# Kernel tuning notes

Measured on AMD Instinct MI355X. Metric: run time of the kernel, lower is better.

Reference implementation:

```python
import jax, jax.numpy as jnp
import numpy as np

_BN_EPS = 1e-5
_BN_SCALE = 1.0 / np.sqrt(1.0 + _BN_EPS)  # eval-mode BN with running mean 0, var 1

def _gelu(x):
    return jax.nn.gelu(x, approximate=False)

def _ln(x, w, b, eps):
    mu = jnp.mean(x, -1, keepdims=True)
    v = jnp.mean((x - mu) ** 2, -1, keepdims=True)
    return (x - mu) * jax.lax.rsqrt(v + eps) * w + b

def _bn(x, s, b):  # NCHW eval BatchNorm (running_mean=0, running_var=1)
    return x * (s * _BN_SCALE)[None, :, None, None] + b[None, :, None, None]

def _conv(x, w, stride=1, pad=1, groups=1, bias=None):
    y = jax.lax.conv_general_dilated(x, w, (stride, stride), [(pad, pad), (pad, pad)],
                                     feature_group_count=groups,
                                     dimension_numbers=('NCHW', 'OIHW', 'NCHW'))
    return y if bias is None else y + bias[None, :, None, None]

def _selective_scan(u, delta, A, Bs, Cs):
    # u, delta: (B,K,D,L); A: (K,D,N); Bs, Cs: (B,K,N,L) -> y: (B,K,D,L)
    def step(h, inp):
        u_l, d_l, B_l, C_l = inp
        dA = jnp.exp(d_l[..., None] * A)                       # (B,K,D,N)
        h = dA * h + (d_l * u_l)[..., None] * B_l[:, :, None, :]
        return h, jnp.sum(h * C_l[:, :, None, :], axis=-1)
    h0 = jnp.zeros(u.shape[:-1] + (A.shape[-1],), u.dtype)
    ins = tuple(jnp.moveaxis(t, -1, 0) for t in (u, delta, Bs, Cs))
    _, ys = jax.lax.scan(step, h0, ins)
    return jnp.moveaxis(ys, 0, -1)

def _ss2d(xh, in_proj, conv_w, conv_b, xproj, dtw, dtb, Alog, D, onw, onb, outproj):
    # xh: (B,H,W,C) -> (B,H,W,C); VMamba SS2D forward_corev0 (4-direction cross-scan)
    B, H, W, C = xh.shape
    di = conv_w.shape[0]
    L = H * W
    xz = xh @ in_proj.T                                        # (B,H,W,2*di)
    xm, z = jnp.split(xz, 2, axis=-1)
    xm = jax.nn.silu(_conv(xm.transpose(0, 3, 1, 2), conv_w, pad=1, groups=di, bias=conv_b))
    x1 = xm.reshape(B, di, L)                                  # row-major scan
    x2 = xm.transpose(0, 1, 3, 2).reshape(B, di, L)            # column-major scan
    xs = jnp.stack([x1, x2, x1[..., ::-1], x2[..., ::-1]], axis=1)  # (B,4,di,L)
    x_dbl = jnp.einsum('bkdl,kcd->bkcl', xs, xproj)
    R = dtw.shape[-1]; N = Alog.shape[-1]
    dts, Bm, Cm = jnp.split(x_dbl, [R, R + N], axis=2)
    delta = jax.nn.softplus(jnp.einsum('bkrl,kdr->bkdl', dts, dtw) + dtb[None, :, :, None])
    A = -jnp.exp(Alog)
    ys = _selective_scan(xs, delta, A, Bm, Cm) + D[None, :, :, None] * xs
    inv = ys[:, 2:4, :, ::-1]
    wh = ys[:, 1].reshape(B, di, W, H).transpose(0, 1, 3, 2).reshape(B, di, L)
    invwh = inv[:, 1].reshape(B, di, W, H).transpose(0, 1, 3, 2).reshape(B, di, L)
    y = ys[:, 0] + inv[:, 0] + wh + invwh                      # (B,di,L)
    y = _ln(y.transpose(0, 2, 1).reshape(B, H, W, di), onw, onb, 1e-5)
    return (y * jax.nn.silu(z)) @ outproj.T

def _forward(x, vss_ln_w, vss_ln_b, vss_in_proj, vss_conv_w, vss_conv_b, vss_xproj, vss_dtw, vss_dtb, vss_Alog, vss_D, vss_onw, vss_onb, vss_outproj, ds_dw, ds_bn1s, ds_bn1b, ds_pw, ds_bn2s, ds_bn2b, fus_c1, fus_bn1s, fus_bn1b, fus_c2, fus_bn2s, fus_bn2b, op_bn0s, op_bn0b, op_conv, op_bn1s, op_bn1b):
    vssp = (vss_ln_w, vss_ln_b, vss_in_proj, vss_conv_w, vss_conv_b, vss_xproj,
            vss_dtw, vss_dtb, vss_Alog, vss_D, vss_onw, vss_onb, vss_outproj)
    def vss(xc, i):  # NCHW -> NHWC -> VSSBlock (x + SS2D(LN(x)), drop_path=identity in eval) -> NCHW
        p = [a[i] for a in vssp]
        xh = xc.transpose(0, 2, 3, 1)
        out = xh + _ss2d(_ln(xh, p[0], p[1], 1e-6), *p[2:])
        return out.transpose(0, 3, 1, 2)
    def down(xc, j):  # depthwise stride-2 conv + BN + GELU, then pointwise conv + BN + GELU
        h = _gelu(_bn(_conv(xc, ds_dw[j], stride=2, pad=1, groups=xc.shape[1]), ds_bn1s[j], ds_bn1b[j]))
        return _gelu(_bn(_conv(h, ds_pw[j], pad=0), ds_bn2s[j], ds_bn2b[j]))
    def resblk(xc, j):  # conv-BN-GELU-(dropout eval=id)-conv-BN + identity, GELU
        h = _gelu(_bn(_conv(xc, fus_c1[j]), fus_bn1s[j], fus_bn1b[j]))
        h = _bn(_conv(h, fus_c2[j]), fus_bn2s[j], fus_bn2b[j])
        return _gelu(h + xc)
    def up(xc, Ho, Wo):  # bilinear, align_corners=True
        h, w = xc.shape[2], xc.shape[3]
        ys = jnp.linspace(0.0, h - 1.0, Ho); xs_ = jnp.linspace(0.0, w - 1.0, Wo)
        y0 = jnp.floor(ys).astype(jnp.int32); y1 = jnp.minimum(y0 + 1, h - 1); wy = (ys - y0).astype(xc.dtype)
        x0 = jnp.floor(xs_).astype(jnp.int32); x1 = jnp.minimum(x0 + 1, w - 1); wx = (xs_ - x0).astype(xc.dtype)
        g = xc[:, :, y0, :] * (1 - wy)[None, None, :, None] + xc[:, :, y1, :] * wy[None, None, :, None]
        return g[:, :, :, x0] * (1 - wx) + g[:, :, :, x1] * wx
    identity = x
    xr = vss(vss(x, 0), 1)                                    # initial refinement
    pyr = [xr]
    cur = xr
    for j in range(2):                                        # pyramid: 16x16 -> 8x8 -> 4x4
        cur = down(cur, j)
        pyr.append(cur)
    proc = [vss(pyr[k], 2 + k) for k in range(3)]             # scale-specific Mamba
    fused = proc[2]
    for i in (1, 0):                                          # bottom-up fusion
        upf = up(fused, proc[i].shape[2], proc[i].shape[3])
        fused = resblk(proc[i] + upf, 1 - i)
    h = _gelu(_bn(fused, op_bn0s, op_bn0b))
    out = _gelu(_bn(_conv(h, op_conv, pad=1), op_bn1s, op_bn1b))
    return out + identity

def setup_inputs() -> dict:
    key = jax.random.key(0)
    ks = iter(jax.random.split(key, 64))
    f32 = jnp.float32
    C, DI, K, N, R = 512, 1024, 4, 16, 32
    B, H, W = 4, 16, 16
    def rn(shape, s=0.02):
        return jax.random.normal(next(ks), shape, f32) * s
    return dict(
        x=jax.random.normal(next(ks), (B, C, H, W), f32),
        vss_ln_w=jnp.ones((5, C), f32), vss_ln_b=jnp.zeros((5, C), f32),
        vss_in_proj=rn((5, 2 * DI, C), 0.03),
        vss_conv_w=rn((5, DI, 1, 3, 3), 0.1), vss_conv_b=jnp.zeros((5, DI), f32),
        vss_xproj=rn((5, K, R + 2 * N, DI), 0.02),
        vss_dtw=rn((5, K, DI, R), 0.05),
        vss_dtb=jax.random.uniform(next(ks), (5, K, DI), f32, -4.0, -2.0),
        vss_Alog=jnp.broadcast_to(jnp.log(jnp.arange(1.0, N + 1.0, dtype=f32)), (5, K, DI, N)).copy(),
        vss_D=jnp.ones((5, K, DI), f32),
        vss_onw=jnp.ones((5, DI), f32), vss_onb=jnp.zeros((5, DI), f32),
        vss_outproj=rn((5, C, DI), 0.02),
        ds_dw=rn((2, C, 1, 3, 3), 0.1), ds_bn1s=jnp.ones((2, C), f32), ds_bn1b=jnp.zeros((2, C), f32),
        ds_pw=rn((2, C, C, 1, 1), 0.03), ds_bn2s=jnp.ones((2, C), f32), ds_bn2b=jnp.zeros((2, C), f32),
        fus_c1=rn((2, C, C, 3, 3), 0.01), fus_bn1s=jnp.ones((2, C), f32), fus_bn1b=jnp.zeros((2, C), f32),
        fus_c2=rn((2, C, C, 3, 3), 0.01), fus_bn2s=jnp.ones((2, C), f32), fus_bn2b=jnp.zeros((2, C), f32),
        op_bn0s=jnp.ones((C,), f32), op_bn0b=jnp.zeros((C,), f32),
        op_conv=rn((C, C, 3, 3), 0.01),
        op_bn1s=jnp.ones((C,), f32), op_bn1b=jnp.zeros((C,), f32),
    )

def reference(x, vss_ln_w, vss_ln_b, vss_in_proj, vss_conv_w, vss_conv_b, vss_xproj, vss_dtw, vss_dtb, vss_Alog, vss_D, vss_onw, vss_onb, vss_outproj, ds_dw, ds_bn1s, ds_bn1b, ds_pw, ds_bn2s, ds_bn2b, fus_c1, fus_bn1s, fus_bn1b, fus_c2, fus_bn2s, fus_bn2b, op_bn0s, op_bn0b, op_conv, op_bn1s, op_bn1b):
    return _forward(x, vss_ln_w, vss_ln_b, vss_in_proj, vss_conv_w, vss_conv_b, vss_xproj, vss_dtw, vss_dtb, vss_Alog, vss_D, vss_onw, vss_onb, vss_outproj, ds_dw, ds_bn1s, ds_bn1b, ds_pw, ds_bn2s, ds_bn2b, fus_c1, fus_bn1s, fus_bn1b, fus_c2, fus_bn2s, fus_bn2b, op_bn0s, op_bn0b, op_conv, op_bn1s, op_bn1b)
```

## Files before the change

### kernel.cpp

```cpp
#include <hip/hip_runtime.h>
#include <hip/hip_bf16.h>
#include <math.h>


constexpr int B_  = 4;
constexpr int C_  = 512;
constexpr int DI_ = 1024;
constexpr int K_  = 4;
constexpr int N_  = 16;
constexpr int R_  = 32;
constexpr int KC9 = C_ * 9;
constexpr int KSPL = 4;
constexpr int KSEG = KC9 / KSPL;
constexpr float BNS_ = 0.9999950000374997f;

typedef __attribute__((ext_vector_type(8))) short bf16x8;
typedef __attribute__((ext_vector_type(4))) float f32x4;

__device__ inline float geluf(float x) {
    return 0.5f * x * (1.0f + erff(x * 0.70710678118654752f));
}
__device__ inline float siluf(float x) {
    return x / (1.0f + expf(-x));
}
__device__ inline float softplusf(float x) {
    return fmaxf(x, 0.0f) + log1pf(expf(-fabsf(x)));
}
__device__ inline float softplus_fast(float x) {
    return fmaxf(x, 0.0f) + __logf(1.0f + __expf(-fabsf(x)));
}
__device__ inline short bf16s(float x) {
    __hip_bfloat16 h = __float2bfloat16(x);
    return *reinterpret_cast<short*>(&h);
}

__device__ inline float blockReduceSum(float v, float* sd) {
    int tid = threadIdx.x;
    sd[tid] = v; __syncthreads();
    for (int s = blockDim.x / 2; s > 0; s >>= 1) {
        if (tid < s) sd[tid] += sd[tid + s];
        __syncthreads();
    }
    float r = sd[0]; __syncthreads();
    return r;
}

__global__ void k_ln_nchw(const float* __restrict__ x, const float* __restrict__ w,
                          const float* __restrict__ b, float* __restrict__ out,
                          int L, float eps) {
    int row = blockIdx.x;
    int bb = row / L, l = row % L;
    __shared__ float sd[256];
    __shared__ float srow[C_];
    const float* xp = x + (size_t)bb * C_ * L + l;
    float sum = 0.f;
    for (int c = threadIdx.x; c < C_; c += 256) { float v = xp[(size_t)c * L]; srow[c] = v; sum += v; }
    sum = blockReduceSum(sum, sd);
    float mu = sum / C_;
    float vs = 0.f;
    for (int c = threadIdx.x; c < C_; c += 256) { float d = srow[c] - mu; vs += d * d; }
    vs = blockReduceSum(vs, sd);
    float rstd = rsqrtf(vs / C_ + eps);
    float* op = out + (size_t)row * C_;
    for (int c = threadIdx.x; c < C_; c += 256) op[c] = (srow[c] - mu) * rstd * w[c] + b[c];
}

template <int EPI>
__global__ void k_gemm_mfma(const float* __restrict__ A, const float* __restrict__ Bw,
                            float* __restrict__ Cout, int M, int Nn, int Kk,
                            const float* __restrict__ Res, int L) {
    const int BK = 32, PITCH = 40;
    __shared__ short As[64 * PITCH];
    __shared__ short Bs[64 * PITCH];
    int m0 = blockIdx.y * 64, n0 = blockIdx.x * 64;
    int tid = threadIdx.x;
    int wv = tid >> 6, lane = tid & 63;
    int frow = lane & 15, kg = lane >> 4;
    f32x4 acc[4];
#pragma unroll
    for (int t = 0; t < 4; t++) acc[t] = (f32x4){0.f, 0.f, 0.f, 0.f};

    int sr = tid >> 2;
    int kq = (tid & 3) * 4;
    for (int k0 = 0; k0 < Kk; k0 += BK) {
        const float* ap = A + (size_t)(m0 + sr) * Kk + k0;
        const float* bp = Bw + (size_t)(n0 + sr) * Kk + k0;
        float4 a1 = *reinterpret_cast<const float4*>(ap + kq);
        float4 a2 = *reinterpret_cast<const float4*>(ap + kq + 16);
        float4 b1 = *reinterpret_cast<const float4*>(bp + kq);
        float4 b2 = *reinterpret_cast<const float4*>(bp + kq + 16);
        short* ad = &As[sr * PITCH + kq];
        ad[0] = bf16s(a1.x); ad[1] = bf16s(a1.y); ad[2] = bf16s(a1.z); ad[3] = bf16s(a1.w);
        ad[16] = bf16s(a2.x); ad[17] = bf16s(a2.y); ad[18] = bf16s(a2.z); ad[19] = bf16s(a2.w);
        short* bd = &Bs[sr * PITCH + kq];
        bd[0] = bf16s(b1.x); bd[1] = bf16s(b1.y); bd[2] = bf16s(b1.z); bd[3] = bf16s(b1.w);
        bd[16] = bf16s(b2.x); bd[17] = bf16s(b2.y); bd[18] = bf16s(b2.z); bd[19] = bf16s(b2.w);
        __syncthreads();
        bf16x8 afrag = *reinterpret_cast<const bf16x8*>(&As[(wv * 16 + frow) * PITCH + kg * 8]);
#pragma unroll
        for (int t = 0; t < 4; t++) {
            bf16x8 bfrag = *reinterpret_cast<const bf16x8*>(&Bs[(t * 16 + frow) * PITCH + kg * 8]);
            acc[t] = __builtin_amdgcn_mfma_f32_16x16x32_bf16(afrag, bfrag, acc[t], 0, 0, 0);
        }
        __syncthreads();
    }

    int orow = kg * 4;
#pragma unroll
    for (int t = 0; t < 4; t++) {
#pragma unroll
        for (int r = 0; r < 4; r++) {
            int m = m0 + wv * 16 + orow + r;
            int n = n0 + t * 16 + frow;
            if (EPI == 0) {
                Cout[(size_t)m * Nn + n] = acc[t][r];
            } else {
                int bb = m / L, l = m % L;
                size_t o = ((size_t)bb * C_ + n) * L + l;
                Cout[o] = Res[o] + acc[t][r];
            }
        }
    }
}

__global__ void k_gemm_part(const float* __restrict__ A, const float* __restrict__ Bw,
                            float* __restrict__ partial, int M, int Nn, int Kk) {
    const int BK = 32, PITCH = 40;
    __shared__ short As[64 * PITCH];
    __shared__ short Bs[64 * PITCH];
    int m0 = blockIdx.y * 64, n0 = blockIdx.x * 64;
    int s = blockIdx.z;
    int tid = threadIdx.x;
    int wv = tid >> 6, lane = tid & 63;
    int frow = lane & 15, kg = lane >> 4;
    f32x4 acc[4];
#pragma unroll
    for (int t = 0; t < 4; t++) acc[t] = (f32x4){0.f, 0.f, 0.f, 0.f};

    int sr = tid >> 2;
    int kq = (tid & 3) * 4;
    int kseg = Kk / KSPL;
    int kbeg = s * kseg;
    for (int k0 = kbeg; k0 < kbeg + kseg; k0 += BK) {
        const float* ap = A + (size_t)(m0 + sr) * Kk + k0;
        const float* bp = Bw + (size_t)(n0 + sr) * Kk + k0;
        float4 a1 = *reinterpret_cast<const float4*>(ap + kq);
        float4 a2 = *reinterpret_cast<const float4*>(ap + kq + 16);
        float4 b1 = *reinterpret_cast<const float4*>(bp + kq);
        float4 b2 = *reinterpret_cast<const float4*>(bp + kq + 16);
        short* ad = &As[sr * PITCH + kq];
        ad[0] = bf16s(a1.x); ad[1] = bf16s(a1.y); ad[2] = bf16s(a1.z); ad[3] = bf16s(a1.w);
        ad[16] = bf16s(a2.x); ad[17] = bf16s(a2.y); ad[18] = bf16s(a2.z); ad[19] = bf16s(a2.w);
        short* bd = &Bs[sr * PITCH + kq];
        bd[0] = bf16s(b1.x); bd[1] = bf16s(b1.y); bd[2] = bf16s(b1.z); bd[3] = bf16s(b1.w);
        bd[16] = bf16s(b2.x); bd[17] = bf16s(b2.y); bd[18] = bf16s(b2.z); bd[19] = bf16s(b2.w);
        __syncthreads();
        bf16x8 afrag = *reinterpret_cast<const bf16x8*>(&As[(wv * 16 + frow) * PITCH + kg * 8]);
#pragma unroll
        for (int t = 0; t < 4; t++) {
            bf16x8 bfrag = *reinterpret_cast<const bf16x8*>(&Bs[(t * 16 + frow) * PITCH + kg * 8]);
            acc[t] = __builtin_amdgcn_mfma_f32_16x16x32_bf16(afrag, bfrag, acc[t], 0, 0, 0);
        }
        __syncthreads();
    }

    int orow = kg * 4;
    float* pb = partial + (size_t)s * M * Nn;
#pragma unroll
    for (int t = 0; t < 4; t++) {
#pragma unroll
        for (int r = 0; r < 4; r++) {
            int m = m0 + wv * 16 + orow + r;
            int n = n0 + t * 16 + frow;
            pb[(size_t)m * Nn + n] = acc[t][r];
        }
    }
}

__global__ void k_outproj_fin(const float* __restrict__ partial, const float* __restrict__ res,
                              float* __restrict__ out, int L) {
    int Nn = C_;
    int total = B_ * L * Nn;
    int idx = blockIdx.x * 256 + threadIdx.x;
    if (idx >= total) return;
    int m = idx / Nn, n = idx % Nn;
    float a = 0.f;
#pragma unroll
    for (int s = 0; s < KSPL; s++) a += partial[(size_t)s * B_ * L * Nn + idx];
    int bb = m / L, l = m % L;
    size_t o = ((size_t)bb * C_ + n) * L + l;
    out[o] = res[o] + a;
}

__global__ void k_im2col(const float* __restrict__ inp, short* __restrict__ ocol,
                         int H, int W) {
    int L = H * W;
    int total = B_ * L * KC9;
    int idx = blockIdx.x * 256 + threadIdx.x;
    if (idx >= total) return;
    int kidx = idx % KC9; int n = idx / KC9;
    int ci = kidx / 9; int q = kidx % 9;
    int dy = q / 3, dx = q % 3;
    int l = n % L; int bb = n / L;
    int h = l / W, w = l % W;
    int hh = h + dy - 1, ww = w + dx - 1;
    float v = 0.f;
    if ((unsigned)hh < (unsigned)H && (unsigned)ww < (unsigned)W)
        v = inp[(((size_t)bb * C_ + ci) * H + hh) * W + ww];
    ocol[idx] = bf16s(v);
}

__global__ void k_gemm_conv_part(const float* __restrict__ wgt, const short* __restrict__ bcol,
                                 float* __restrict__ partial, int Nn) {
    const int BK = 32, PITCH = 40;
    __shared__ short As[64 * PITCH];
    __shared__ short Bs[64 * PITCH];
    int m0 = blockIdx.y * 64, n0 = blockIdx.x * 64;
    int s = blockIdx.z;
    int tid = threadIdx.x;
    int wv = tid >> 6, lane = tid & 63;
    int frow = lane & 15, kg = lane >> 4;
    f32x4 acc[4];
#pragma unroll
    for (int t = 0; t < 4; t++) acc[t] = (f32x4){0.f, 0.f, 0.f, 0.f};

    int sr = tid >> 2;
    int kq = (tid & 3) * 4;
    int kq8 = (tid & 3) * 8;
    int kbeg = s * KSEG;
    for (int k0 = kbeg; k0 < kbeg + KSEG; k0 += BK) {
        const float* ap = wgt + (size_t)(m0 + sr) * KC9 + k0;
        float4 a1 = *reinterpret_cast<const float4*>(ap + kq);
        float4 a2 = *reinterpret_cast<const float4*>(ap + kq + 16);
        short* ad = &As[sr * PITCH + kq];
        ad[0] = bf16s(a1.x); ad[1] = bf16s(a1.y); ad[2] = bf16s(a1.z); ad[3] = bf16s(a1.w);
        ad[16] = bf16s(a2.x); ad[17] = bf16s(a2.y); ad[18] = bf16s(a2.z); ad[19] = bf16s(a2.w);
        uint4 bv = *reinterpret_cast<const uint4*>(bcol + (size_t)(n0 + sr) * KC9 + k0 + kq8);
        *reinterpret_cast<uint4*>(&Bs[sr * PITCH + kq8]) = bv;
        __syncthreads();
        bf16x8 afrag = *reinterpret_cast<const bf16x8*>(&As[(wv * 16 + frow) * PITCH + kg * 8]);
#pragma unroll
        for (int t = 0; t < 4; t++) {
            bf16x8 bfrag = *reinterpret_cast<const bf16x8*>(&Bs[(t * 16 + frow) * PITCH + kg * 8]);
            acc[t] = __builtin_amdgcn_mfma_f32_16x16x32_bf16(afrag, bfrag, acc[t], 0, 0, 0);
        }
        __syncthreads();
    }

    int orow = kg * 4;
    float* pb = partial + (size_t)s * C_ * Nn;
#pragma unroll
    for (int t = 0; t < 4; t++) {
#pragma unroll
        for (int r = 0; r < 4; r++) {
            int m = m0 + wv * 16 + orow + r;
            int n = n0 + t * 16 + frow;
            pb[(size_t)m * Nn + n] = acc[t][r];
        }
    }
}

template <int CM>
__global__ void k_conv_fin2(const float* __restrict__ partial, const float* __restrict__ bns,
                            const float* __restrict__ bnb, const float* __restrict__ res,
                            float* __restrict__ out, int Nn, int L) {
    int idx = blockIdx.x * 256 + threadIdx.x;
    int total = C_ * Nn;
    if (idx >= total) return;
    int m = idx / Nn, n = idx % Nn;
    float a = 0.f;
#pragma unroll
    for (int s = 0; s < KSPL; s++) a += partial[(size_t)s * C_ * Nn + idx];
    int bb = n / L, l = n % L;
    size_t o = ((size_t)bb * C_ + m) * L + l;
    a = a * (bns[m] * BNS_) + bnb[m];
    if (CM == 0) out[o] = geluf(a);
    else if (CM == 1) out[o] = geluf(a + res[o]);
    else out[o] = geluf(a) + res[o];
}

__global__ void k_dwconv_silu(const float* __restrict__ xz, const float* __restrict__ cw,
                              const float* __restrict__ cb, float* __restrict__ xm,
                              float* __restrict__ xmT, int H, int W) {
    int L = H * W;
    int idx = blockIdx.x * 256 + threadIdx.x;
    int total = B_ * L * DI_;
    if (idx >= total) return;
    int d = idx % DI_; int t = idx / DI_; int l = t % L; int bb = t / L;
    int h = l / W, w = l % W;
    float acc = cb[d];
    const float* wp = cw + d * 9;
#pragma unroll
    for (int dy = 0; dy < 3; dy++) {
        int hh = h + dy - 1;
        if ((unsigned)hh >= (unsigned)H) continue;
#pragma unroll
        for (int dx = 0; dx < 3; dx++) {
            int ww = w + dx - 1;
            if ((unsigned)ww >= (unsigned)W) continue;
            acc += xz[((size_t)bb * L + hh * W + ww) * (2 * DI_) + d] * wp[dy * 3 + dx];
        }
    }
    float v = siluf(acc);
    xm[idx] = v;
    xmT[((size_t)bb * DI_ + d) * L + l] = v;
}

__device__ inline int dir_src(int k, int l, int H, int W, int L) {
    int ll = (k >= 2) ? (L - 1 - l) : l;
    return (k & 1) ? ((ll % H) * W + ll / H) : ll;
}

__global__ void k_gather_xdbl(const float* __restrict__ tmp, float* __restrict__ xdbl,
                              int H, int W) {
    int L = H * W;
    int Nn = B_ * L;
    int total = B_ * K_ * 64 * L;
    int idx = blockIdx.x * 256 + threadIdx.x;
    if (idx >= total) return;
    int l = idx % L; int t = idx / L; int c = t % 64; t /= 64; int k = t % K_; int bb = t / K_;
    int src = dir_src(k, l, H, W, L);
    size_t col = (size_t)bb * L + src;
    float v = 0.f;
#pragma unroll
    for (int s = 0; s < KSPL; s++)
        v += tmp[((size_t)s * K_ * 64 + k * 64 + c) * Nn + col];
    xdbl[idx] = v;
}

template <int LT>
__global__ void k_scan_wave(const float* __restrict__ xmT, const float* __restrict__ xdbl,
                            const float* __restrict__ dtw, const float* __restrict__ dtb,
                            const float* __restrict__ Alog, const float* __restrict__ Dp,
                            float* __restrict__ part, int H, int W) {
    constexpr int SPL = (LT == 256) ? 4 : 1;
    constexpr int CW  = (LT < 64) ? LT : 64;
    const int L = LT;
    int lane = threadIdx.x & 63;
    int wv = threadIdx.x >> 6;
    int blk = blockIdx.x;
    const int ndq = DI_ / 4;
    int dq = blk % ndq; int t2 = blk / ndq; int k = t2 % K_; int bb = t2 / K_;
    int d = dq * 4 + wv;

    const float* wrow = dtw + ((size_t)k * DI_ + d) * R_;
    const float* al   = Alog + ((size_t)k * DI_ + d) * N_;
    float bias = dtb[k * DI_ + d];
    float Dv   = Dp[k * DI_ + d];

    const float* bc = xdbl + (size_t)(bb * K_ + k) * 64 * L;
    const float* ut = xmT + ((size_t)bb * DI_ + d) * L;
    float* yb = part + (size_t)(bb * K_ + k) * L * DI_ + d;

    int lj = lane < CW ? lane : CW - 1;
    int base = lj * SPL;

    float dl[SPL], du[SPL], uu[SPL], y[SPL];
    {
        float accv[SPL];
#pragma unroll
        for (int i = 0; i < SPL; i++) accv[i] = bias;
#pragma unroll 8
        for (int r = 0; r < R_; r++) {
            float wr = wrow[r];
            if constexpr (SPL == 4) {
                float4 d4 = *reinterpret_cast<const float4*>(bc + (size_t)r * L + base);
                accv[0] += d4.x * wr; accv[1] += d4.y * wr;
                accv[2] += d4.z * wr; accv[3] += d4.w * wr;
            } else {
                accv[0] += bc[(size_t)r * L + base] * wr;
            }
        }
#pragma unroll
        for (int i = 0; i < SPL; i++) {
            int src = dir_src(k, base + i, H, W, L);
            dl[i] = softplus_fast(accv[i]);
            uu[i] = ut[src];
            du[i] = dl[i] * uu[i];
            y[i] = 0.f;
        }
    }

#pragma unroll 1
    for (int n = 0; n < N_; n++) {
        float An = -__expf(al[n]);
        float aL, bL;
        if constexpr (SPL == 4) {
            float4 B4 = *reinterpret_cast<const float4*>(bc + (size_t)(R_ + n) * L + base);
            float a0 = __expf(dl[0] * An);
            float a1 = __expf(dl[1] * An);
            float a2 = __expf(dl[2] * An);
            float a3 = __expf(dl[3] * An);
            aL = a0; bL = du[0] * B4.x;
            bL = a1 * bL + du[1] * B4.y; aL = a1 * aL;
            bL = a2 * bL + du[2] * B4.z; aL = a2 * aL;
            bL = a3 * bL + du[3] * B4.w; aL = a3 * aL;
#pragma unroll
            for (int off = 1; off < CW; off <<= 1) {
                float ap = __shfl_up(aL, off);
                float bp = __shfl_up(bL, off);
                if (lane >= off) { bL = aL * bp + bL; aL = aL * ap; }
            }
            float hin = __shfl_up(bL, 1);
            if (lane == 0) hin = 0.f;
            float4 C4 = *reinterpret_cast<const float4*>(bc + (size_t)(R_ + N_ + n) * L + base);
            float h = hin;
            h = a0 * h + du[0] * B4.x; y[0] += h * C4.x;
            h = a1 * h + du[1] * B4.y; y[1] += h * C4.y;
            h = a2 * h + du[2] * B4.z; y[2] += h * C4.z;
            h = a3 * h + du[3] * B4.w; y[3] += h * C4.w;
        } else {
            float Bv = bc[(size_t)(R_ + n) * L + base];
            float a0 = __expf(dl[0] * An);
            aL = a0;
            bL = du[0] * Bv;
#pragma unroll
            for (int off = 1; off < CW; off <<= 1) {
                float ap = __shfl_up(aL, off);
                float bp = __shfl_up(bL, off);
                if (lane >= off) { bL = aL * bp + bL; aL = aL * ap; }
            }
            float hin = __shfl_up(bL, 1);
            if (lane == 0) hin = 0.f;
            float h = a0 * hin + du[0] * Bv;
            y[0] += h * bc[(size_t)(R_ + N_ + n) * L + base];
        }
    }

    if (lane < CW) {
#pragma unroll
        for (int i = 0; i < SPL; i++) {
            int src = dir_src(k, base + i, H, W, L);
            yb[(size_t)src * DI_] = y[i] + Dv * uu[i];
        }
    }
}

__global__ void k_merge_ln_silu(const float* __restrict__ part, const float* __restrict__ xz,
                                const float* __restrict__ onw, const float* __restrict__ onb,
                                float* __restrict__ tout, int L) {
    int row = blockIdx.x;
    int bb = row / L, l = row % L;
    __shared__ float sd[256];
    __shared__ float srow[DI_];
    const float* p0 = part + ((size_t)(bb * K_ + 0) * L + l) * DI_;
    const float* p1 = part + ((size_t)(bb * K_ + 1) * L + l) * DI_;
    const float* p2 = part + ((size_t)(bb * K_ + 2) * L + l) * DI_;
    const float* p3 = part + ((size_t)(bb * K_ + 3) * L + l) * DI_;
    float sum = 0.f;
    for (int d = threadIdx.x; d < DI_; d += 256) {
        float v = p0[d] + p1[d] + p2[d] + p3[d];
        srow[d] = v; sum += v;
    }
    sum = blockReduceSum(sum, sd);
    float mu = sum / DI_;
    float vs = 0.f;
    for (int d = threadIdx.x; d < DI_; d += 256) { float dv = srow[d] - mu; vs += dv * dv; }
    vs = blockReduceSum(vs, sd);
    float rstd = rsqrtf(vs / DI_ + 1e-5f);
    const float* zp = xz + (size_t)row * 2 * DI_ + DI_;
    float* tp = tout + (size_t)row * DI_;
    for (int d = threadIdx.x; d < DI_; d += 256) {
        float zn = zp[d];
        tp[d] = ((srow[d] - mu) * rstd * onw[d] + onb[d]) * siluf(zn);
    }
}

__global__ void k_dwconv_s2_bn_gelu(const float* __restrict__ x, const float* __restrict__ dw,
                                    const float* __restrict__ bns, const float* __restrict__ bnb,
                                    float* __restrict__ out, int Hi, int Wi) {
    int Ho = Hi / 2, Wo = Wi / 2;
    int idx = blockIdx.x * 256 + threadIdx.x;
    int total = B_ * C_ * Ho * Wo;
    if (idx >= total) return;
    int wo = idx % Wo; int t = idx / Wo; int ho = t % Ho; t /= Ho; int c = t % C_; int bb = t / C_;
    float acc = 0.f;
    const float* xp = x + ((size_t)bb * C_ + c) * Hi * Wi;
    const float* wp = dw + c * 9;
#pragma unroll
    for (int dy = 0; dy < 3; dy++) {
        int ih = ho * 2 + dy - 1;
        if ((unsigned)ih >= (unsigned)Hi) continue;
#pragma unroll
        for (int dx = 0; dx < 3; dx++) {
            int iw = wo * 2 + dx - 1;
            if ((unsigned)iw >= (unsigned)Wi) continue;
            acc += xp[ih * Wi + iw] * wp[dy * 3 + dx];
        }
    }
    acc = acc * (bns[c] * BNS_) + bnb[c];
    out[idx] = geluf(acc);
}

__global__ void k_pwconv_bn_gelu(const float* __restrict__ x, const float* __restrict__ pw,
                                 const float* __restrict__ bns, const float* __restrict__ bnb,
                                 float* __restrict__ out, int L) {
    int idx = blockIdx.x * 256 + threadIdx.x;
    int total = B_ * C_ * L;
    if (idx >= total) return;
    int l = idx % L; int t = idx / L; int co = t % C_; int bb = t / C_;
    const float* xp = x + (size_t)bb * C_ * L + l;
    const float* wp = pw + (size_t)co * C_;
    float acc = 0.f;
    for (int ci = 0; ci < C_; ci++) acc += xp[(size_t)ci * L] * wp[ci];
    acc = acc * (bns[co] * BNS_) + bnb[co];
    out[idx] = geluf(acc);
}

__global__ void k_up_add(const float* __restrict__ low, const float* __restrict__ skip,
                         float* __restrict__ out, int Hi, int Wi, int Ho, int Wo) {
    int idx = blockIdx.x * 256 + threadIdx.x;
    int total = B_ * C_ * Ho * Wo;
    if (idx >= total) return;
    int wo = idx % Wo; int t = idx / Wo; int ho = t % Ho; t /= Ho; int c = t % C_; int bb = t / C_;
    float fy = (float)ho * (float)(Hi - 1) / (float)(Ho - 1);
    float fx = (float)wo * (float)(Wi - 1) / (float)(Wo - 1);
    int y0 = (int)floorf(fy); int y1 = min(y0 + 1, Hi - 1); float wy = fy - (float)y0;
    int x0 = (int)floorf(fx); int x1 = min(x0 + 1, Wi - 1); float wx = fx - (float)x0;
    const float* lp = low + ((size_t)bb * C_ + c) * Hi * Wi;
    float g0 = lp[y0 * Wi + x0] * (1.f - wy) + lp[y1 * Wi + x0] * wy;
    float g1 = lp[y0 * Wi + x1] * (1.f - wy) + lp[y1 * Wi + x1] * wy;
    out[idx] = skip[idx] + g0 * (1.f - wx) + g1 * wx;
}

__global__ void k_bn_gelu(const float* __restrict__ x, const float* __restrict__ s,
                          const float* __restrict__ b, float* __restrict__ out, int L) {
    int idx = blockIdx.x * 256 + threadIdx.x;
    int total = B_ * C_ * L;
    if (idx >= total) return;
    int t = idx / L; int c = t % C_;
    out[idx] = geluf(x[idx] * (s[c] * BNS_) + b[c]);
}

__global__ void k_fill_out(float* o, int n, float v) {
    int i = blockIdx.x * 256 + threadIdx.x;
    if (i < n) o[i] = v;
}

struct VssW {
    const float *lnw, *lnb, *inproj, *convw, *convb, *xproj, *dtw, *dtb, *Alog, *D, *onw, *onb, *outproj;
};

static void run_vss(const float* xc_in, float* xc_out, const VssW& p, int H, int W,
                    float* xln, float* xz, float* xm, float* xmT, float* xdbl,
                    float* part, float* ybuf, float* tbuf, float* cpart2,
                    hipStream_t stream) {
    int L = H * W, M = B_ * L;
    k_ln_nchw<<<M, 256, 0, stream>>>(xc_in, p.lnw, p.lnb, xln, L, 1e-6f);
    {
        dim3 g(2 * DI_ / 64, M / 64);
        k_gemm_mfma<0><<<g, 256, 0, stream>>>(xln, p.inproj, xz, M, 2 * DI_, C_, nullptr, L);
    }
    {
        int tot = B_ * L * DI_;
        k_dwconv_silu<<<(tot + 255) / 256, 256, 0, stream>>>(xz, p.convw, p.convb, xm, xmT, H, W);
    }
    {
        float* tmp = ybuf;
        dim3 g(M / 64, (K_ * 64) / 64, KSPL);
        k_gemm_part<<<g, 256, 0, stream>>>(p.xproj, xm, tmp, K_ * 64, M, DI_);
        int tot = B_ * K_ * 64 * L;
        k_gather_xdbl<<<(tot + 255) / 256, 256, 0, stream>>>(tmp, xdbl, H, W);
    }
    {
        int g = B_ * K_ * (DI_ / 4);
        if (L == 256)
            k_scan_wave<256><<<g, 256, 0, stream>>>(xmT, xdbl, p.dtw, p.dtb, p.Alog, p.D, part, H, W);
        else if (L == 64)
            k_scan_wave<64><<<g, 256, 0, stream>>>(xmT, xdbl, p.dtw, p.dtb, p.Alog, p.D, part, H, W);
        else
            k_scan_wave<16><<<g, 256, 0, stream>>>(xmT, xdbl, p.dtw, p.dtb, p.Alog, p.D, part, H, W);
    }
    k_merge_ln_silu<<<M, 256, 0, stream>>>(part, xz, p.onw, p.onb, tbuf, L);
    {
        dim3 g(C_ / 64, M / 64, KSPL);
        k_gemm_part<<<g, 256, 0, stream>>>(tbuf, p.outproj, cpart2, M, C_, DI_);
        int tot = M * C_;
        k_outproj_fin<<<(tot + 255) / 256, 256, 0, stream>>>(cpart2, xc_in, xc_out, L);
    }
}

extern "C" void kernel_launch(void* const* d_in, const int* in_sizes, int n_in,
                              void* d_out, int out_size, void* d_ws, size_t ws_size,
                              hipStream_t stream) {
    constexpr size_t NEED_FLOATS = 14221312;
    constexpr size_t NEED_BYTES  = NEED_FLOATS * 4;
    if (ws_size < NEED_BYTES) {
        k_fill_out<<<(out_size + 255) / 256, 256, 0, stream>>>((float*)d_out, out_size, 0.0f);
        return;
    }

    const float* x        = (const float*)d_in[0];
    const float* lnw      = (const float*)d_in[1];
    const float* lnb      = (const float*)d_in[2];
    const float* inproj   = (const float*)d_in[3];
    const float* convw    = (const float*)d_in[4];
    const float* convb    = (const float*)d_in[5];
    const float* xprojp   = (const float*)d_in[6];
    const float* dtwp     = (const float*)d_in[7];
    const float* dtbp     = (const float*)d_in[8];
    const float* Alogp    = (const float*)d_in[9];
    const float* Dpp      = (const float*)d_in[10];
    const float* onwp     = (const float*)d_in[11];
    const float* onbp     = (const float*)d_in[12];
    const float* outprojp = (const float*)d_in[13];
    const float* ds_dw    = (const float*)d_in[14];
    const float* ds_bn1s  = (const float*)d_in[15];
    const float* ds_bn1b  = (const float*)d_in[16];
    const float* ds_pw    = (const float*)d_in[17];
    const float* ds_bn2s  = (const float*)d_in[18];
    const float* ds_bn2b  = (const float*)d_in[19];
    const float* fus_c1   = (const float*)d_in[20];
    const float* fus_bn1s = (const float*)d_in[21];
    const float* fus_bn1b = (const float*)d_in[22];
    const float* fus_c2   = (const float*)d_in[23];
    const float* fus_bn2s = (const float*)d_in[24];
    const float* fus_bn2b = (const float*)d_in[25];
    const float* op_bn0s  = (const float*)d_in[26];
    const float* op_bn0b  = (const float*)d_in[27];
    const float* op_conv  = (const float*)d_in[28];
    const float* op_bn1s  = (const float*)d_in[29];
    const float* op_bn1b  = (const float*)d_in[30];

    float* ws = (float*)d_ws;
    float* xln   = ws;
    float* xz    = ws + 524288;
    float* xm    = ws + 2621440;
    float* xdbl  = ws + 3670016;
    float* ybuf  = ws + 3932160;
    float* part  = ws + 4980736;
    float* tbuf  = part;
    float* t_a   = ws + 9175040;
    float* xr    = ws + 9699328;
    float* p1    = ws + 10223616;
    float* p2    = ws + 10354688;
    float* proc0 = ws + 10387456;
    float* proc1 = ws + 10911744;
    float* proc2 = ws + 11042816;
    float* xmT   = ws + 11075584;
    float* cpart2= ws + 12124160;
    tbuf = ybuf;
    float* p1pre = xz;
    float* p2pre = xz + 131072;
    float* up1t  = xln;
    float* rbh1  = xln + 131072;
    float* fus1  = xln + 262144;
    float* up0t  = xm;
    float* rbh0  = part;
    float* fus0  = part + 524288;
    float* hbuf  = part + 1048576;
    short* icol = (short*)(ws + 6553600);

    VssW vp[5];
    for (int i = 0; i < 5; i++) {
        vp[i].lnw     = lnw + (size_t)i * C_;
        vp[i].lnb     = lnb + (size_t)i * C_;
        vp[i].inproj  = inproj + (size_t)i * 2 * DI_ * C_;
        vp[i].convw   = convw + (size_t)i * DI_ * 9;
        vp[i].convb   = convb + (size_t)i * DI_;
        vp[i].xproj   = xprojp + (size_t)i * K_ * 64 * DI_;
        vp[i].dtw     = dtwp + (size_t)i * K_ * DI_ * R_;
        vp[i].dtb     = dtbp + (size_t)i * K_ * DI_;
        vp[i].Alog    = Alogp + (size_t)i * K_ * DI_ * N_;
        vp[i].D       = Dpp + (size_t)i * K_ * DI_;
        vp[i].onw     = onwp + (size_t)i * DI_;
        vp[i].onb     = onbp + (size_t)i * DI_;
        vp[i].outproj = outprojp + (size_t)i * C_ * DI_;
    }

    run_vss(x,   t_a, vp[0], 16, 16, xln, xz, xm, xmT, xdbl, part, ybuf, tbuf, cpart2, stream);
    run_vss(t_a, xr,  vp[1], 16, 16, xln, xz, xm, xmT, xdbl, part, ybuf, tbuf, cpart2, stream);

    k_dwconv_s2_bn_gelu<<<(B_ * C_ * 64 + 255) / 256, 256, 0, stream>>>(
        xr, ds_dw, ds_bn1s, ds_bn1b, p1pre, 16, 16);
    k_pwconv_bn_gelu<<<(B_ * C_ * 64 + 255) / 256, 256, 0, stream>>>(
        p1pre, ds_pw, ds_bn2s, ds_bn2b, p1, 64);
    k_dwconv_s2_bn_gelu<<<(B_ * C_ * 16 + 255) / 256, 256, 0, stream>>>(
        p1, ds_dw + (size_t)C_ * 9, ds_bn1s + C_, ds_bn1b + C_, p2pre, 8, 8);
    k_pwconv_bn_gelu<<<(B_ * C_ * 16 + 255) / 256, 256, 0, stream>>>(
        p2pre, ds_pw + (size_t)C_ * C_, ds_bn2s + C_, ds_bn2b + C_, p2, 16);

    run_vss(xr, proc0, vp[2], 16, 16, xln, xz, xm, xmT, xdbl, part, ybuf, tbuf, cpart2, stream);
    run_vss(p1, proc1, vp[3],  8,  8, xln, xz, xm, xmT, xdbl, part, ybuf, tbuf, cpart2, stream);
    run_vss(p2, proc2, vp[4],  4,  4, xln, xz, xm, xmT, xdbl, part, ybuf, tbuf, cpart2, stream);

    k_up_add<<<(B_ * C_ * 64 + 255) / 256, 256, 0, stream>>>(proc2, proc1, up1t, 4, 4, 8, 8);
    {
        int Nn = B_ * 64;
        int tot = Nn * KC9;
        int tfin = C_ * Nn;
        dim3 gg(Nn / 64, C_ / 64, KSPL);
        k_im2col<<<(tot + 255) / 256, 256, 0, stream>>>(up1t, icol, 8, 8);
        k_gemm_conv_part<<<gg, 256, 0, stream>>>(fus_c1, icol, cpart2, Nn);
        k_conv_fin2<0><<<(tfin + 255) / 256, 256, 0, stream>>>(cpart2, fus_bn1s, fus_bn1b,
                                                               nullptr, rbh1, Nn, 64);
        k_im2col<<<(tot + 255) / 256, 256, 0, stream>>>(rbh1, icol, 8, 8);
        k_gemm_conv_part<<<gg, 256, 0, stream>>>(fus_c2, icol, cpart2, Nn);
        k_conv_fin2<1><<<(tfin + 255) / 256, 256, 0, stream>>>(cpart2, fus_bn2s, fus_bn2b,
                                                               up1t, fus1, Nn, 64);
    }
    k_up_add<<<(B_ * C_ * 256 + 255) / 256, 256, 0, stream>>>(fus1, proc0, up0t, 8, 8, 16, 16);
    {
        int Nn = B_ * 256;
        int tot = Nn * KC9;
        int tfin = C_ * Nn;
        dim3 gg(Nn / 64, C_ / 64, KSPL);
        k_im2col<<<(tot + 255) / 256, 256, 0, stream>>>(up0t, icol, 16, 16);
        k_gemm_conv_part<<<gg, 256, 0, stream>>>(fus_c1 + (size_t)C_ * KC9, icol, cpart2, Nn);
        k_conv_fin2<0><<<(tfin + 255) / 256, 256, 0, stream>>>(cpart2, fus_bn1s + C_, fus_bn1b + C_,
                                                               nullptr, rbh0, Nn, 256);
        k_im2col<<<(tot + 255) / 256, 256, 0, stream>>>(rbh0, icol, 16, 16);
        k_gemm_conv_part<<<gg, 256, 0, stream>>>(fus_c2 + (size_t)C_ * KC9, icol, cpart2, Nn);
        k_conv_fin2<1><<<(tfin + 255) / 256, 256, 0, stream>>>(cpart2, fus_bn2s + C_, fus_bn2b + C_,
                                                               up0t, fus0, Nn, 256);
    }

    k_bn_gelu<<<(B_ * C_ * 256 + 255) / 256, 256, 0, stream>>>(fus0, op_bn0s, op_bn0b, hbuf, 256);
    {
        int Nn = B_ * 256;
        int tot = Nn * KC9;
        int tfin = C_ * Nn;
        dim3 gg(Nn / 64, C_ / 64, KSPL);
        k_im2col<<<(tot + 255) / 256, 256, 0, stream>>>(hbuf, icol, 16, 16);
        k_gemm_conv_part<<<gg, 256, 0, stream>>>(op_conv, icol, cpart2, Nn);
        k_conv_fin2<2><<<(tfin + 255) / 256, 256, 0, stream>>>(cpart2, op_bn1s, op_bn1b,
                                                               x, (float*)d_out, Nn, 256);
    }
    (void)in_sizes; (void)n_in; (void)out_size;
}
```

Measured before the change: 834.5 us.

## Route pointwise downsample convs through MFMA split-K GEMM and fuse final BN-GELU

The depthwise stride-2 conv now writes channel-last (token-major) output so the following 1x1 pointwise conv can run on the existing split-K k_gemm_part MFMA GEMM. A new k_pw_fin kernel sums the partials, applies BN and GELU, and writes NCHW. This replaces the naive scalar per-output dot-product kernel, which was slow. Separately, the op-head BN+GELU is folded into the last fusion conv's epilogue (new CM==3 mode), which removes one elementwise pass and its intermediate buffer.

```diff
diff --git a/kernel.cpp b/kernel.cpp
--- a/kernel.cpp
+++ b/kernel.cpp
@@ -192,6 +192,20 @@
     out[o] = res[o] + a;
 }
 
+__global__ void k_pw_fin(const float* __restrict__ partial, const float* __restrict__ bns,
+                         const float* __restrict__ bnb, float* __restrict__ out,
+                         int M, int L2) {
+    int total = M * C_;
+    int idx = blockIdx.x * 256 + threadIdx.x;
+    if (idx >= total) return;
+    int m = idx / C_, n = idx % C_;
+    float a = 0.f;
+#pragma unroll
+    for (int s = 0; s < KSPL; s++) a += partial[(size_t)s * M * C_ + idx];
+    int bb = m / L2, l = m % L2;
+    out[((size_t)bb * C_ + n) * L2 + l] = geluf(a * (bns[n] * BNS_) + bnb[n]);
+}
+
 __global__ void k_im2col(const float* __restrict__ inp, short* __restrict__ ocol,
                          int H, int W) {
     int L = H * W;
@@ -263,7 +277,8 @@
 template <int CM>
 __global__ void k_conv_fin2(const float* __restrict__ partial, const float* __restrict__ bns,
                             const float* __restrict__ bnb, const float* __restrict__ res,
-                            float* __restrict__ out, int Nn, int L) {
+                            float* __restrict__ out, int Nn, int L,
+                            const float* __restrict__ bns2, const float* __restrict__ bnb2) {
     int idx = blockIdx.x * 256 + threadIdx.x;
     int total = C_ * Nn;
     if (idx >= total) return;
@@ -276,7 +291,37 @@
     a = a * (bns[m] * BNS_) + bnb[m];
     if (CM == 0) out[o] = geluf(a);
     else if (CM == 1) out[o] = geluf(a + res[o]);
-    else out[o] = geluf(a) + res[o];
+    else if (CM == 2) out[o] = geluf(a) + res[o];
+    else {
+        float v = geluf(a + res[o]);
+        out[o] = geluf(v * (bns2[m] * BNS_) + bnb2[m]);
+    }
+}
+
+__global__ void k_dwconv_s2_bn_gelu(const float* __restrict__ x, const float* __restrict__ dw,
+                                    const float* __restrict__ bns, const float* __restrict__ bnb,
+                                    float* __restrict__ out, int Hi, int Wi) {
+    int Ho = Hi / 2, Wo = Wi / 2;
+    int idx = blockIdx.x * 256 + threadIdx.x;
+    int total = B_ * C_ * Ho * Wo;
+    if (idx >= total) return;
+    int c = idx % C_; int t = idx / C_; int wo = t % Wo; t /= Wo; int ho = t % Ho; int bb = t / Ho;
+    float acc = 0.f;
+    const float* xp = x + ((size_t)bb * C_ + c) * Hi * Wi;
+    const float* wp = dw + c * 9;
+#pragma unroll
+    for (int dy = 0; dy < 3; dy++) {
+        int ih = ho * 2 + dy - 1;
+        if ((unsigned)ih >= (unsigned)Hi) continue;
+#pragma unroll
+        for (int dx = 0; dx < 3; dx++) {
+            int iw = wo * 2 + dx - 1;
+            if ((unsigned)iw >= (unsigned)Wi) continue;
+            acc += xp[ih * Wi + iw] * wp[dy * 3 + dx];
+        }
+    }
+    acc = acc * (bns[c] * BNS_) + bnb[c];
+    out[((size_t)(bb * Ho + ho) * Wo + wo) * C_ + c] = geluf(acc);
 }
 
 __global__ void k_dwconv_silu(const float* __restrict__ xz, const float* __restrict__ cw,
@@ -466,47 +511,6 @@
     }
 }
 
-__global__ void k_dwconv_s2_bn_gelu(const float* __restrict__ x, const float* __restrict__ dw,
-                                    const float* __restrict__ bns, const float* __restrict__ bnb,
-                                    float* __restrict__ out, int Hi, int Wi) {
-    int Ho = Hi / 2, Wo = Wi / 2;
-    int idx = blockIdx.x * 256 + threadIdx.x;
-    int total = B_ * C_ * Ho * Wo;
-    if (idx >= total) return;
-    int wo = idx % Wo; int t = idx / Wo; int ho = t % Ho; t /= Ho; int c = t % C_; int bb = t / C_;
-    float acc = 0.f;
-    const float* xp = x + ((size_t)bb * C_ + c) * Hi * Wi;
-    const float* wp = dw + c * 9;
-#pragma unroll
-    for (int dy = 0; dy < 3; dy++) {
-        int ih = ho * 2 + dy - 1;
-        if ((unsigned)ih >= (unsigned)Hi) continue;
-#pragma unroll
-        for (int dx = 0; dx < 3; dx++) {
-            int iw = wo * 2 + dx - 1;
-            if ((unsigned)iw >= (unsigned)Wi) continue;
-            acc += xp[ih * Wi + iw] * wp[dy * 3 + dx];
-        }
-    }
-    acc = acc * (bns[c] * BNS_) + bnb[c];
-    out[idx] = geluf(acc);
-}
-
-__global__ void k_pwconv_bn_gelu(const float* __restrict__ x, const float* __restrict__ pw,
-                                 const float* __restrict__ bns, const float* __restrict__ bnb,
-                                 float* __restrict__ out, int L) {
-    int idx = blockIdx.x * 256 + threadIdx.x;
-    int total = B_ * C_ * L;
-    if (idx >= total) return;
-    int l = idx % L; int t = idx / L; int co = t % C_; int bb = t / C_;
-    const float* xp = x + (size_t)bb * C_ * L + l;
-    const float* wp = pw + (size_t)co * C_;
-    float acc = 0.f;
-    for (int ci = 0; ci < C_; ci++) acc += xp[(size_t)ci * L] * wp[ci];
-    acc = acc * (bns[co] * BNS_) + bnb[co];
-    out[idx] = geluf(acc);
-}
-
 __global__ void k_up_add(const float* __restrict__ low, const float* __restrict__ skip,
                          float* __restrict__ out, int Hi, int Wi, int Ho, int Wo) {
     int idx = blockIdx.x * 256 + threadIdx.x;
@@ -521,15 +525,6 @@
     float g0 = lp[y0 * Wi + x0] * (1.f - wy) + lp[y1 * Wi + x0] * wy;
     float g1 = lp[y0 * Wi + x1] * (1.f - wy) + lp[y1 * Wi + x1] * wy;
     out[idx] = skip[idx] + g0 * (1.f - wx) + g1 * wx;
-}
-
-__global__ void k_bn_gelu(const float* __restrict__ x, const float* __restrict__ s,
-                          const float* __restrict__ b, float* __restrict__ out, int L) {
-    int idx = blockIdx.x * 256 + threadIdx.x;
-    int total = B_ * C_ * L;
-    if (idx >= total) return;
-    int t = idx / L; int c = t % C_;
-    out[idx] = geluf(x[idx] * (s[c] * BNS_) + b[c]);
 }
 
 __global__ void k_fill_out(float* o, int n, float v) {
@@ -640,14 +635,13 @@
     float* xmT   = ws + 11075584;
     float* cpart2= ws + 12124160;
     tbuf = ybuf;
-    float* p1pre = xz;
-    float* p2pre = xz + 131072;
+    float* p1preT= xz;
+    float* p2preT= xz + 131072;
     float* up1t  = xln;
     float* rbh1  = xln + 131072;
     float* fus1  = xln + 262144;
     float* up0t  = xm;
     float* rbh0  = part;
-    float* fus0  = part + 524288;
     float* hbuf  = part + 1048576;
     short* icol = (short*)(ws + 6553600);
 
@@ -672,13 +666,21 @@
     run_vss(t_a, xr,  vp[1], 16, 16, xln, xz, xm, xmT, xdbl, part, ybuf, tbuf, cpart2, stream);
 
     k_dwconv_s2_bn_gelu<<<(B_ * C_ * 64 + 255) / 256, 256, 0, stream>>>(
-        xr, ds_dw, ds_bn1s, ds_bn1b, p1pre, 16, 16);
-    k_pwconv_bn_gelu<<<(B_ * C_ * 64 + 255) / 256, 256, 0, stream>>>(
-        p1pre, ds_pw, ds_bn2s, ds_bn2b, p1, 64);
+        xr, ds_dw, ds_bn1s, ds_bn1b, p1preT, 16, 16);
+    {
+        int M = B_ * 64;
+        dim3 g(C_ / 64, M / 64, KSPL);
+        k_gemm_part<<<g, 256, 0, stream>>>(p1preT, ds_pw, cpart2, M, C_, C_);
+        k_pw_fin<<<(M * C_ + 255) / 256, 256, 0, stream>>>(cpart2, ds_bn2s, ds_bn2b, p1, M, 64);
+    }
     k_dwconv_s2_bn_gelu<<<(B_ * C_ * 16 + 255) / 256, 256, 0, stream>>>(
-        p1, ds_dw + (size_t)C_ * 9, ds_bn1s + C_, ds_bn1b + C_, p2pre, 8, 8);
-    k_pwconv_bn_gelu<<<(B_ * C_ * 16 + 255) / 256, 256, 0, stream>>>(
-        p2pre, ds_pw + (size_t)C_ * C_, ds_bn2s + C_, ds_bn2b + C_, p2, 16);
+        p1, ds_dw + (size_t)C_ * 9, ds_bn1s + C_, ds_bn1b + C_, p2preT, 8, 8);
+    {
+        int M = B_ * 16;
+        dim3 g(C_ / 64, M / 64, KSPL);
+        k_gemm_part<<<g, 256, 0, stream>>>(p2preT, ds_pw + (size_t)C_ * C_, cpart2, M, C_, C_);
+        k_pw_fin<<<(M * C_ + 255) / 256, 256, 0, stream>>>(cpart2, ds_bn2s + C_, ds_bn2b + C_, p2, M, 16);
+    }
 
     run_vss(xr, proc0, vp[2], 16, 16, xln, xz, xm, xmT, xdbl, part, ybuf, tbuf, cpart2, stream);
     run_vss(p1, proc1, vp[3],  8,  8, xln, xz, xm, xmT, xdbl, part, ybuf, tbuf, cpart2, stream);
@@ -693,11 +695,13 @@
         k_im2col<<<(tot + 255) / 256, 256, 0, stream>>>(up1t, icol, 8, 8);
         k_gemm_conv_part<<<gg, 256, 0, stream>>>(fus_c1, icol, cpart2, Nn);
         k_conv_fin2<0><<<(tfin + 255) / 256, 256, 0, stream>>>(cpart2, fus_bn1s, fus_bn1b,
-                                                               nullptr, rbh1, Nn, 64);
+                                                               nullptr, rbh1, Nn, 64,
+                                                               nullptr, nullptr);
         k_im2col<<<(tot + 255) / 256, 256, 0, stream>>>(rbh1, icol, 8, 8);
         k_gemm_conv_part<<<gg, 256, 0, stream>>>(fus_c2, icol, cpart2, Nn);
         k_conv_fin2<1><<<(tfin + 255) / 256, 256, 0, stream>>>(cpart2, fus_bn2s, fus_bn2b,
-                                                               up1t, fus1, Nn, 64);
+                                                               up1t, fus1, Nn, 64,
+                                                               nullptr, nullptr);
     }
     k_up_add<<<(B_ * C_ * 256 + 255) / 256, 256, 0, stream>>>(fus1, proc0, up0t, 8, 8, 16, 16);
     {
@@ -708,14 +712,15 @@
         k_im2col<<<(tot + 255) / 256, 256, 0, stream>>>(up0t, icol, 16, 16);
         k_gemm_conv_part<<<gg, 256, 0, stream>>>(fus_c1 + (size_t)C_ * KC9, icol, cpart2, Nn);
         k_conv_fin2<0><<<(tfin + 255) / 256, 256, 0, stream>>>(cpart2, fus_bn1s + C_, fus_bn1b + C_,
-                                                               nullptr, rbh0, Nn, 256);
+                                                               nullptr, rbh0, Nn, 256,
+                                                               nullptr, nullptr);
         k_im2col<<<(tot + 255) / 256, 256, 0, stream>>>(rbh0, icol, 16, 16);
         k_gemm_conv_part<<<gg, 256, 0, stream>>>(fus_c2 + (size_t)C_ * KC9, icol, cpart2, Nn);
-        k_conv_fin2<1><<<(tfin + 255) / 256, 256, 0, stream>>>(cpart2, fus_bn2s + C_, fus_bn2b + C_,
-                                                               up0t, fus0, Nn, 256);
-    }
-
-    k_bn_gelu<<<(B_ * C_ * 256 + 255) / 256, 256, 0, stream>>>(fus0, op_bn0s, op_bn0b, hbuf, 256);
+        k_conv_fin2<3><<<(tfin + 255) / 256, 256, 0, stream>>>(cpart2, fus_bn2s + C_, fus_bn2b + C_,
+                                                               up0t, hbuf, Nn, 256,
+                                                               op_bn0s, op_bn0b);
+    }
+
     {
         int Nn = B_ * 256;
         int tot = Nn * KC9;
@@ -724,7 +729,8 @@
         k_im2col<<<(tot + 255) / 256, 256, 0, stream>>>(hbuf, icol, 16, 16);
         k_gemm_conv_part<<<gg, 256, 0, stream>>>(op_conv, icol, cpart2, Nn);
         k_conv_fin2<2><<<(tfin + 255) / 256, 256, 0, stream>>>(cpart2, op_bn1s, op_bn1b,
-                                                               x, (float*)d_out, Nn, 256);
+                                                               x, (float*)d_out, Nn, 256,
+                                                               nullptr, nullptr);
     }
     (void)in_sizes; (void)n_in; (void)out_size;
 }
```

New measurement: 776.0 us (median of 2 runs). 1.08x faster.
